# Kernel optimization log

Hardware: AMD Instinct MI355X
Metric: run time of the kernel (lower is better)

## Reference

```python
import jax, jax.numpy as jnp
import numpy as np

WS = 7
NUM_HEADS = 4
DIM = 128


def _ln(x, g, b, eps=1e-5):
    m = x.mean(-1, keepdims=True)
    v = ((x - m) ** 2).mean(-1, keepdims=True)
    return (x - m) / jnp.sqrt(v + eps) * g + b


def _rel_index(ws):
    # (N, N) relative-position index into the (2*ws-1)^2 bias table
    coords = np.stack(np.meshgrid(np.arange(ws), np.arange(ws), indexing='ij')).reshape(2, -1)
    rel = (coords[:, :, None] - coords[:, None, :]).transpose(1, 2, 0)
    rel[..., 0] += ws - 1
    rel[..., 1] += ws - 1
    rel[..., 0] *= 2 * ws - 1
    return rel.sum(-1)


def _attn_mask(Hp, Wp, ws):
    # (nW, N, N) additive shift mask, -100 where tokens come from different regions
    shift = ws // 2
    img = np.zeros((Hp, Wp))
    slices = (slice(0, -ws), slice(-ws, -shift), slice(-shift, None))
    cnt = 0
    for sh in slices:
        for sw in slices:
            img[sh, sw] = cnt
            cnt += 1
    mw = img.reshape(Hp // ws, ws, Wp // ws, ws).transpose(0, 2, 1, 3).reshape(-1, ws * ws)
    diff = mw[:, None, :] - mw[:, :, None]
    return np.where(diff != 0, -100.0, 0.0).astype(np.float32)


def setup_inputs() -> dict:
    key = jax.random.key(0)
    ks = jax.random.split(key, 8)
    d, h, ws = DIM, 4 * DIM, WS
    B, H, W = 64, 56, 56

    def w(k, shape, s=0.02):
        return (jax.random.normal(k, shape) * s).astype(jnp.float32)

    return {
        'x': jax.random.normal(ks[0], (B, H * W, d), jnp.float32),
        'norm1_g': jnp.ones(d, jnp.float32), 'norm1_b': jnp.zeros(d, jnp.float32),
        'qkv_w': w(ks[1], (d, 3 * d)), 'qkv_b': jnp.zeros(3 * d, jnp.float32),
        'proj_w': w(ks[2], (d, d)), 'proj_b': jnp.zeros(d, jnp.float32),
        'rpb_table': w(ks[3], ((2 * ws - 1) ** 2, NUM_HEADS)),
        'norm2_g': jnp.ones(d, jnp.float32), 'norm2_b': jnp.zeros(d, jnp.float32),
        'fc1_w': w(ks[4], (d, h)), 'fc1_b': jnp.zeros(h, jnp.float32),
        'fc2_w': w(ks[5], (h, d)), 'fc2_b': jnp.zeros(d, jnp.float32),
        'H': H, 'W': W,
    }


def reference(x, norm1_g, norm1_b, qkv_w, qkv_b, proj_w, proj_b, rpb_table,
              norm2_g, norm2_b, fc1_w, fc1_b, fc2_w, fc2_b, H, W):
    ws, nh = WS, NUM_HEADS
    B, L, C = x.shape
    d_head = C // nh
    scale = d_head ** -0.5
    shift = ws // 2
    N = ws * ws

    shortcut = x
    xn = _ln(x, norm1_g, norm1_b).reshape(B, H, W, C)
    pad_b = (ws - H % ws) % ws
    pad_r = (ws - W % ws) % ws
    if pad_b or pad_r:
        xn = jnp.pad(xn, ((0, 0), (0, pad_b), (0, pad_r), (0, 0)))
    Hp, Wp = H + pad_b, W + pad_r

    # cyclic shift (shift=True branch)
    xn = jnp.roll(xn, (-shift, -shift), axis=(1, 2))

    # window partition: (B, Hp, Wp, C) -> (B*nW, N, C)
    nHw, nWw = Hp // ws, Wp // ws
    win = xn.reshape(B, nHw, ws, nWw, ws, C).transpose(0, 1, 3, 2, 4, 5).reshape(B * nHw * nWw, N, C)

    qkv = (win @ qkv_w + qkv_b).reshape(-1, N, 3, nh, d_head).transpose(2, 0, 3, 1, 4)
    q, k, v = qkv[0], qkv[1], qkv[2]  # (Bw, nh, N, d_head)

    attn = jnp.einsum('bhnd,bhmd->bhnm', q, k) * scale
    bias = rpb_table[jnp.asarray(_rel_index(ws))].transpose(2, 0, 1)  # (nh, N, N)
    attn = attn + bias[None]

    mask = jnp.asarray(_attn_mask(Hp, Wp, ws))  # (nW, N, N)
    nW = mask.shape[0]
    attn = attn.reshape(B, nW, nh, N, N) + mask[None, :, None]
    attn = jax.nn.softmax(attn.reshape(-1, nh, N, N), axis=-1)

    out = jnp.einsum('bhnm,bhmd->bhnd', attn, v).transpose(0, 2, 1, 3).reshape(-1, N, C)
    out = out @ proj_w + proj_b

    # window reverse + un-shift + un-pad
    out = out.reshape(B, nHw, nWw, ws, ws, C).transpose(0, 1, 3, 2, 4, 5).reshape(B, Hp, Wp, C)
    out = jnp.roll(out, (shift, shift), axis=(1, 2))
    out = out[:, :H, :W].reshape(B, H * W, C) + shortcut

    out = out + (jax.nn.gelu(_ln(out, norm2_g, norm2_b) @ fc1_w + fc1_b, approximate=False) @ fc2_w + fc2_b)
    return out
```

## Files before the change

kernel.cpp:

```cpp
#include <hip/hip_runtime.h>
#include <hip/hip_bf16.h>
#include <math.h>

typedef __bf16 bf16x8 __attribute__((ext_vector_type(8)));
typedef __bf16 bf16x4 __attribute__((ext_vector_type(4)));
typedef float  f32x4  __attribute__((ext_vector_type(4)));
typedef unsigned int u32x4 __attribute__((ext_vector_type(4)));
typedef __hip_bfloat16 bf16_t;

static constexpr int C_    = 128;
static constexpr int L_    = 56 * 56;
static constexpr int M_    = 64 * L_;
static constexpr int NWIN  = 64 * 64;

__device__ inline long win_to_tok(int tw)
{
    int win = tw / 49, n = tw % 49;
    int bb  = win >> 6, wi = win & 63;
    int wh  = wi >> 3, wwp = wi & 7;
    int hs  = wh * 7 + n / 7;
    int wsv = wwp * 7 + n % 7;
    int hh  = (hs + 3) % 56;
    int ww  = (wsv + 3) % 56;
    return (long)bb * L_ + hh * 56 + ww;
}

__device__ inline unsigned int pk2(float lo, float hi)
{
    unsigned short a = __builtin_bit_cast(unsigned short, (__bf16)lo);
    unsigned short b = __builtin_bit_cast(unsigned short, (__bf16)hi);
    return (unsigned int)a | ((unsigned int)b << 16);
}

__device__ inline float gelu_f(float x)
{
    float u = 0.7978845608f * x * (1.f + 0.044715f * x * x);
    float e = __expf(2.f * fminf(u, 15.f));
    return x * e * __builtin_amdgcn_rcpf(e + 1.f);
}

__global__ void sentinel_kernel(float* o) { o[threadIdx.x] = 1e9f; }

__global__ void transpose_w(const float* __restrict__ w, bf16_t* __restrict__ wt,
                            int K, int N)
{
    int i = blockIdx.x * 256 + threadIdx.x;
    if (i >= K * N) return;
    int k = i / N, n = i % N;
    wt[(long)n * K + k] = __float2bfloat16(w[i]);
}

__global__ __launch_bounds__(256) void swin_fused(const float* __restrict__ x,
                                                  const float* __restrict__ lng,
                                                  const float* __restrict__ lnb,
                                                  const bf16_t* __restrict__ qkvwt,
                                                  const float*  __restrict__ qkvb,
                                                  const float*  __restrict__ rpb,
                                                  const bf16_t* __restrict__ projwt,
                                                  const float*  __restrict__ projb,
                                                  bf16_t* __restrict__ y)
{
    __shared__ char smem[16384 + 32768 + 14336];
    char*   xnb = smem;
    char*   qkb = smem + 16384;
    __bf16* vtb = (__bf16*)(smem + 49152);

    int win  = blockIdx.x;
    int tid  = threadIdx.x;
    int wave = tid >> 6;
    int lane = tid & 63;
    int la = lane & 15, lb = lane >> 4;

    for (int i = tid; i < 128 * 7; i += 256)
        vtb[(i / 7) * 56 + 49 + i % 7] = (__bf16)0.f;

    {
        int row = wave * 16 + la;
        int tw  = win * 49 + row;
        if (tw > M_ - 1) tw = M_ - 1;
        long src = win_to_tok(tw);
        const float* xr = x + src * C_;
        float vals[4][8];
        float sm = 0.f, qs = 0.f;
#pragma unroll
        for (int kt = 0; kt < 4; ++kt) {
            f32x4 u0 = *reinterpret_cast<const f32x4*>(xr + kt * 32 + lb * 8);
            f32x4 u1 = *reinterpret_cast<const f32x4*>(xr + kt * 32 + lb * 8 + 4);
#pragma unroll
            for (int j = 0; j < 4; ++j) { vals[kt][j] = u0[j]; vals[kt][4 + j] = u1[j]; }
#pragma unroll
            for (int j = 0; j < 8; ++j) { sm += vals[kt][j]; qs += vals[kt][j] * vals[kt][j]; }
        }
        sm += __shfl_xor(sm, 16); sm += __shfl_xor(sm, 32);
        qs += __shfl_xor(qs, 16); qs += __shfl_xor(qs, 32);
        float mean = sm * (1.f / 128.f);
        float rstd = rsqrtf(qs * (1.f / 128.f) - mean * mean + 1e-5f);
#pragma unroll
        for (int kt = 0; kt < 4; ++kt) {
            bf16x8 v8;
#pragma unroll
            for (int j = 0; j < 8; ++j) {
                int col = kt * 32 + lb * 8 + j;
                v8[j] = (__bf16)((vals[kt][j] - mean) * rstd * lng[col] + lnb[col]);
            }
            int colb = kt * 64 + lb * 16;
            *reinterpret_cast<bf16x8*>(xnb + row * 256 + (colb ^ ((row & 7) << 4))) = v8;
        }
    }
    __syncthreads();

    {
        int c0 = wave * 96;
        f32x4 acc[4][6];
#pragma unroll
        for (int nt = 0; nt < 6; ++nt) {
            float bv = qkvb[c0 + nt * 16 + la];
#pragma unroll
            for (int s = 0; s < 4; ++s) acc[s][nt] = (f32x4){bv, bv, bv, bv};
        }
#pragma unroll
        for (int kt = 0; kt < 4; ++kt) {
            bf16x8 ar[4];
#pragma unroll
            for (int s = 0; s < 4; ++s) {
                int row = s * 16 + la;
                ar[s] = *reinterpret_cast<const bf16x8*>(
                    xnb + row * 256 + ((kt * 64 + lb * 16) ^ ((row & 7) << 4)));
            }
#pragma unroll
            for (int nt = 0; nt < 6; ++nt) {
                bf16x8 br = *reinterpret_cast<const bf16x8*>(
                    qkvwt + (long)(c0 + nt * 16 + la) * 128 + kt * 32 + lb * 8);
#pragma unroll
                for (int s = 0; s < 4; ++s)
                    acc[s][nt] = __builtin_amdgcn_mfma_f32_16x16x32_bf16(
                        ar[s], br, acc[s][nt], 0, 0, 0);
            }
        }
#pragma unroll
        for (int s = 0; s < 4; ++s) {
#pragma unroll
            for (int r = 0; r < 4; ++r) {
                int row = s * 16 + lb * 4 + r;
#pragma unroll
                for (int nt = 0; nt < 6; ++nt) {
                    int col = c0 + nt * 16 + la;
                    float v = acc[s][nt][r];
                    if (col < 256) {
                        *reinterpret_cast<__bf16*>(
                            qkb + row * 512 + ((col * 2) ^ ((row & 7) << 4))) = (__bf16)v;
                    } else if (row < 49) {
                        vtb[(col - 256) * 56 + row] = (__bf16)v;
                    }
                }
            }
        }
    }
    __syncthreads();

    int h = wave;
    bf16x8 kf[4], qf[4];
#pragma unroll
    for (int t = 0; t < 4; ++t) {
        int row = t * 16 + la;
        kf[t] = *reinterpret_cast<const bf16x8*>(
            qkb + row * 512 + ((256 + h * 64 + lb * 16) ^ ((row & 7) << 4)));
        qf[t] = *reinterpret_cast<const bf16x8*>(
            qkb + row * 512 + ((      h * 64 + lb * 16) ^ ((row & 7) << 4)));
    }

    f32x4 S[4][4];
#pragma unroll
    for (int qt = 0; qt < 4; ++qt)
#pragma unroll
        for (int kt = 0; kt < 4; ++kt)
            S[qt][kt] = __builtin_amdgcn_mfma_f32_16x16x32_bf16(
                kf[kt], qf[qt], (f32x4){0.f, 0.f, 0.f, 0.f}, 0, 0, 0);

    const float scale = 0.17677669529663687f;
    int wi  = win & 63;
    int wh  = wi >> 3, wwp = wi & 7;
    bool edge = (wh == 7) || (wwp == 7);

    int i1[4], j1[4], r1[4], c1[4];
#pragma unroll
    for (int qt = 0; qt < 4; ++qt) {
        int q  = qt * 16 + la;
        int qc = q < 49 ? q : 48;
        i1[qt] = qc / 7; j1[qt] = qc - 7 * i1[qt];
        r1[qt] = (wh  < 7) ? 0 : ((i1[qt] < 4) ? 1 : 2);
        c1[qt] = (wwp < 7) ? 0 : ((j1[qt] < 4) ? 1 : 2);
    }

#pragma unroll
    for (int kt = 0; kt < 4; ++kt) {
#pragma unroll
        for (int r = 0; r < 4; ++r) {
            if (kt == 3 && r > 0) {
#pragma unroll
                for (int qt = 0; qt < 4; ++qt) S[qt][kt][r] = -1e30f;
                continue;
            }
            int key = kt * 16 + lb * 4 + r;
            int kc  = key < 49 ? key : 48;
            int i2  = kc / 7, j2 = kc - 7 * i2;
            int r2  = (wh  < 7) ? 0 : ((i2 < 4) ? 1 : 2);
            int c2  = (wwp < 7) ? 0 : ((j2 < 4) ? 1 : 2);
#pragma unroll
            for (int qt = 0; qt < 4; ++qt) {
                float bv  = rpb[(((i1[qt] - i2 + 6) * 13 + (j1[qt] - j2 + 6)) << 2) + h];
                float val = S[qt][kt][r] * scale + bv;
                if (edge && ((r1[qt] != r2) | (c1[qt] != c2))) val -= 100.f;
                if (kt == 3 && lb > 0) val = -1e30f;
                S[qt][kt][r] = val;
            }
        }
    }

    float inv[4];
#pragma unroll
    for (int qt = 0; qt < 4; ++qt) {
        float mx = -3e38f;
#pragma unroll
        for (int kt = 0; kt < 4; ++kt)
#pragma unroll
            for (int r = 0; r < 4; ++r) mx = fmaxf(mx, S[qt][kt][r]);
        mx = fmaxf(mx, __shfl_xor(mx, 16));
        mx = fmaxf(mx, __shfl_xor(mx, 32));
        float sm = 0.f;
#pragma unroll
        for (int kt = 0; kt < 4; ++kt)
#pragma unroll
            for (int r = 0; r < 4; ++r) {
                float e = __expf(S[qt][kt][r] - mx);
                S[qt][kt][r] = e;
                sm += e;
            }
        sm += __shfl_xor(sm, 16);
        sm += __shfl_xor(sm, 32);
        inv[qt] = 1.f / sm;
    }

    unsigned int w_[4][4][2];
#pragma unroll
    for (int qt = 0; qt < 4; ++qt)
#pragma unroll
        for (int t = 0; t < 4; ++t) {
            w_[qt][t][0] = pk2(S[qt][t][0], S[qt][t][1]);
            w_[qt][t][1] = pk2(S[qt][t][2], S[qt][t][3]);
        }

    int srcA = la + (((2 * lb)     & 3) << 4);
    int srcB = la + (((2 * lb + 1) & 3) << 4);
    bool hiT = (lb >> 1) & 1;

    f32x4 O[2][4];
#pragma unroll
    for (int dt = 0; dt < 2; ++dt)
#pragma unroll
        for (int qt = 0; qt < 4; ++qt) O[dt][qt] = (f32x4){0.f, 0.f, 0.f, 0.f};

#pragma unroll
    for (int kk = 0; kk < 2; ++kk) {
        bf16x8 vf[2];
#pragma unroll
        for (int dt = 0; dt < 2; ++dt)
            vf[dt] = *reinterpret_cast<const bf16x8*>(
                vtb + (h * 32 + dt * 16 + la) * 56 + kk * 32 + lb * 8);
        int tl = kk * 2;
#pragma unroll
        for (int qt = 0; qt < 4; ++qt) {
            unsigned int a0 = __shfl(w_[qt][tl][0],     srcA);
            unsigned int b0 = __shfl(w_[qt][tl + 1][0], srcA);
            unsigned int a1 = __shfl(w_[qt][tl][1],     srcA);
            unsigned int b1 = __shfl(w_[qt][tl + 1][1], srcA);
            unsigned int a2 = __shfl(w_[qt][tl][0],     srcB);
            unsigned int b2 = __shfl(w_[qt][tl + 1][0], srcB);
            unsigned int a3 = __shfl(w_[qt][tl][1],     srcB);
            unsigned int b3 = __shfl(w_[qt][tl + 1][1], srcB);
            u32x4 uu = { hiT ? b0 : a0, hiT ? b1 : a1, hiT ? b2 : a2, hiT ? b3 : a3 };
            bf16x8 pf = __builtin_bit_cast(bf16x8, uu);
#pragma unroll
            for (int dt = 0; dt < 2; ++dt)
                O[dt][qt] = __builtin_amdgcn_mfma_f32_16x16x32_bf16(vf[dt], pf, O[dt][qt], 0, 0, 0);
        }
    }

    __bf16 (*attw)[152] = (__bf16(*)[152])xnb;
#pragma unroll
    for (int qt = 0; qt < 4; ++qt) {
        int q = qt * 16 + la;
        if (q < 49) {
            float iv = inv[qt];
#pragma unroll
            for (int dt = 0; dt < 2; ++dt) {
                unsigned int s0 = pk2(O[dt][qt][0] * iv, O[dt][qt][1] * iv);
                unsigned int s1 = pk2(O[dt][qt][2] * iv, O[dt][qt][3] * iv);
                uint2 st = {s0, s1};
                *reinterpret_cast<uint2*>(&attw[q][h * 32 + dt * 16 + lb * 4]) = st;
            }
        }
    }
    __syncthreads();

    int n0 = h * 32;
    f32x4 pacc[4][2];
#pragma unroll
    for (int nt = 0; nt < 2; ++nt) {
        float bv = projb[n0 + nt * 16 + la];
#pragma unroll
        for (int s = 0; s < 4; ++s) pacc[s][nt] = (f32x4){bv, bv, bv, bv};
    }
#pragma unroll
    for (int kt = 0; kt < 4; ++kt) {
        bf16x8 ar[4];
#pragma unroll
        for (int s = 0; s < 4; ++s)
            ar[s] = *reinterpret_cast<const bf16x8*>(&attw[s * 16 + la][kt * 32 + lb * 8]);
#pragma unroll
        for (int nt = 0; nt < 2; ++nt) {
            bf16x8 br = *reinterpret_cast<const bf16x8*>(
                projwt + (long)(n0 + nt * 16 + la) * 128 + kt * 32 + lb * 8);
#pragma unroll
            for (int s = 0; s < 4; ++s)
                pacc[s][nt] = __builtin_amdgcn_mfma_f32_16x16x32_bf16(
                    ar[s], br, pacc[s][nt], 0, 0, 0);
        }
    }

#pragma unroll
    for (int s = 0; s < 4; ++s) {
#pragma unroll
        for (int r = 0; r < 4; ++r) {
            int q = s * 16 + lb * 4 + r;
            if (q < 49) {
                long to = win_to_tok(win * 49 + q);
#pragma unroll
                for (int nt = 0; nt < 2; ++nt) {
                    int col = n0 + nt * 16 + la;
                    y[to * C_ + col] =
                        __float2bfloat16(pacc[s][nt][r] + x[to * C_ + col]);
                }
            }
        }
    }
}

__global__ __launch_bounds__(512, 4) void mlp_fused(const bf16_t* __restrict__ y,
                                                    const float* __restrict__ g,
                                                    const float* __restrict__ b,
                                                    const bf16_t* __restrict__ w1t,
                                                    const float* __restrict__ b1,
                                                    const bf16_t* __restrict__ w2t,
                                                    const float* __restrict__ b2,
                                                    float* __restrict__ out)
{
    __shared__ uint4 ldsq[2048];
    int tid  = threadIdx.x;
    int lane = tid & 63;
    int la = lane & 15, lb = lane >> 4;
    int m0 = (blockIdx.x * 8 + (tid >> 6)) * 32;

    auto stage = [&](int c) {
        char* d1 = (char*)&ldsq[0];
        const char* s1 = (const char*)w1t + (size_t)c * 16384;
#pragma unroll
        for (int i = 0; i < 2; ++i) {
            int idx = i * 512 + tid;
            int row = idx >> 4, colb = (idx & 15) * 16;
            uint4 v = *reinterpret_cast<const uint4*>(s1 + idx * 16);
            *reinterpret_cast<uint4*>(d1 + row * 256 + (colb ^ ((row & 7) << 4))) = v;
        }
        char* d2 = (char*)&ldsq[1024];
        const char* s2 = (const char*)w2t + (size_t)c * 128;
#pragma unroll
        for (int i = 0; i < 2; ++i) {
            int idx = i * 512 + tid;
            int row = idx >> 3, colb = (idx & 7) * 16;
            uint4 v = *reinterpret_cast<const uint4*>(s2 + (size_t)row * 1024 + colb);
            *reinterpret_cast<uint4*>(d2 + row * 128 + (colb ^ ((row & 7) << 4))) = v;
        }
    };

    bf16x8 af[2][4];
#pragma unroll
    for (int s = 0; s < 2; ++s) {
        const bf16_t* yr = y + (long)(m0 + s * 16 + la) * C_;
        float vals[4][8];
        float sm = 0.f, qs = 0.f;
#pragma unroll
        for (int kt = 0; kt < 4; ++kt) {
            bf16x8 v8 = *reinterpret_cast<const bf16x8*>(yr + kt * 32 + lb * 8);
#pragma unroll
            for (int j = 0; j < 8; ++j) {
                float v = (float)v8[j];
                vals[kt][j] = v; sm += v; qs += v * v;
            }
        }
        sm += __shfl_xor(sm, 16); sm += __shfl_xor(sm, 32);
        qs += __shfl_xor(qs, 16); qs += __shfl_xor(qs, 32);
        float mean = sm * (1.f / 128.f);
        float rstd = rsqrtf(qs * (1.f / 128.f) - mean * mean + 1e-5f);
#pragma unroll
        for (int kt = 0; kt < 4; ++kt)
#pragma unroll
            for (int j = 0; j < 8; ++j) {
                int col = kt * 32 + lb * 8 + j;
                af[s][kt][j] = (__bf16)((vals[kt][j] - mean) * rstd * g[col] + b[col]);
            }
    }

    f32x4 acc[2][8];
#pragma unroll
    for (int nt2 = 0; nt2 < 8; ++nt2) {
        f32x4 bv = *reinterpret_cast<const f32x4*>(b2 + nt2 * 16 + lb * 4);
#pragma unroll
        for (int s = 0; s < 2; ++s) acc[s][nt2] = bv;
    }

    int srcA = la + (((2 * lb)     & 3) << 4);
    int srcB = la + (((2 * lb + 1) & 3) << 4);
    bool hiT = (lb >> 1) & 1;

    for (int c = 0; c < 8; ++c) {
        stage(c);
        __syncthreads();

        const char* L1 = (const char*)&ldsq[0];
        const char* L2 = (const char*)&ldsq[1024];

        f32x4 hacc[2][4];
#pragma unroll
        for (int nt = 0; nt < 4; ++nt) {
            f32x4 bv = *reinterpret_cast<const f32x4*>(b1 + c * 64 + nt * 16 + lb * 4);
#pragma unroll
            for (int s = 0; s < 2; ++s) hacc[s][nt] = bv;
        }
#pragma unroll
        for (int kt = 0; kt < 4; ++kt)
#pragma unroll
            for (int nt = 0; nt < 4; ++nt) {
                int row = nt * 16 + la;
                bf16x8 w1f = *reinterpret_cast<const bf16x8*>(
                    L1 + row * 256 + ((kt * 64 + lb * 16) ^ ((row & 7) << 4)));
#pragma unroll
                for (int s = 0; s < 2; ++s)
                    hacc[s][nt] = __builtin_amdgcn_mfma_f32_16x16x32_bf16(
                        w1f, af[s][kt], hacc[s][nt], 0, 0, 0);
            }
        unsigned int wpk[2][4][2];
#pragma unroll
        for (int s = 0; s < 2; ++s)
#pragma unroll
            for (int t = 0; t < 4; ++t) {
                f32x4 hv = hacc[s][t];
#pragma unroll
                for (int r = 0; r < 4; ++r) hv[r] = gelu_f(hv[r]);
                wpk[s][t][0] = pk2(hv[0], hv[1]);
                wpk[s][t][1] = pk2(hv[2], hv[3]);
            }
#pragma unroll
        for (int kk = 0; kk < 2; ++kk) {
            int tl = kk * 2;
#pragma unroll
            for (int s = 0; s < 2; ++s) {
                unsigned int a0 = __shfl(wpk[s][tl][0],     srcA);
                unsigned int b0 = __shfl(wpk[s][tl + 1][0], srcA);
                unsigned int a1 = __shfl(wpk[s][tl][1],     srcA);
                unsigned int b1v = __shfl(wpk[s][tl + 1][1], srcA);
                unsigned int a2 = __shfl(wpk[s][tl][0],     srcB);
                unsigned int b2v = __shfl(wpk[s][tl + 1][0], srcB);
                unsigned int a3 = __shfl(wpk[s][tl][1],     srcB);
                unsigned int b3v = __shfl(wpk[s][tl + 1][1], srcB);
                u32x4 uu = { hiT ? b0 : a0, hiT ? b1v : a1, hiT ? b2v : a2, hiT ? b3v : a3 };
                bf16x8 pf = __builtin_bit_cast(bf16x8, uu);
#pragma unroll
                for (int nt2 = 0; nt2 < 8; ++nt2) {
                    int row2 = nt2 * 16 + la;
                    bf16x8 w2f = *reinterpret_cast<const bf16x8*>(
                        L2 + row2 * 128 + ((kk * 64 + lb * 16) ^ ((row2 & 7) << 4)));
                    acc[s][nt2] = __builtin_amdgcn_mfma_f32_16x16x32_bf16(
                        w2f, pf, acc[s][nt2], 0, 0, 0);
                }
            }
        }
        __syncthreads();
    }

#pragma unroll
    for (int s = 0; s < 2; ++s) {
        long m = m0 + s * 16 + la;
        const bf16_t* yrow = y + m * C_;
        float* orow = out + m * C_;
#pragma unroll
        for (int nt2 = 0; nt2 < 8; ++nt2) {
            int n2 = nt2 * 16 + lb * 4;
            bf16x4 rb = *reinterpret_cast<const bf16x4*>(yrow + n2);
            f32x4 val = acc[s][nt2];
#pragma unroll
            for (int r = 0; r < 4; ++r) val[r] += (float)rb[r];
            *reinterpret_cast<f32x4*>(orow + n2) = val;
        }
    }
}

extern "C" void kernel_launch(void* const* d_in, const int* in_sizes, int n_in,
                              void* d_out, int out_size, void* d_ws, size_t ws_size,
                              hipStream_t stream)
{
    (void)in_sizes; (void)n_in; (void)out_size;

    const float* x      = (const float*)d_in[0];
    const float* n1g    = (const float*)d_in[1];
    const float* n1b    = (const float*)d_in[2];
    const float* qkv_w  = (const float*)d_in[3];
    const float* qkv_b  = (const float*)d_in[4];
    const float* proj_w = (const float*)d_in[5];
    const float* proj_b = (const float*)d_in[6];
    const float* rpb    = (const float*)d_in[7];
    const float* n2g    = (const float*)d_in[8];
    const float* n2b    = (const float*)d_in[9];
    const float* fc1_w  = (const float*)d_in[10];
    const float* fc1_b  = (const float*)d_in[11];
    const float* fc2_w  = (const float*)d_in[12];
    const float* fc2_b  = (const float*)d_in[13];

    char* ws = (char*)d_ws;

    const size_t yb_sz = (size_t)M_ * 128 * 2;
    const size_t w_sz  = (size_t)(128 * 384 + 128 * 128 + 128 * 512 + 512 * 128) * 2;
    const size_t need  = yb_sz + w_sz;

    if (need > ws_size) {
        sentinel_kernel<<<1, 256, 0, stream>>>((float*)d_out);
        return;
    }

    bf16_t* yb      = (bf16_t*)ws;
    bf16_t* qkv_wt  = (bf16_t*)(ws + yb_sz);
    bf16_t* proj_wt = qkv_wt + 128 * 384;
    bf16_t* fc1_wt  = proj_wt + 128 * 128;
    bf16_t* fc2_wt  = fc1_wt + 128 * 512;

    transpose_w<<<(128 * 384 + 255) / 256, 256, 0, stream>>>(qkv_w, qkv_wt, 128, 384);
    transpose_w<<<(128 * 128 + 255) / 256, 256, 0, stream>>>(proj_w, proj_wt, 128, 128);
    transpose_w<<<(128 * 512 + 255) / 256, 256, 0, stream>>>(fc1_w, fc1_wt, 128, 512);
    transpose_w<<<(512 * 128 + 255) / 256, 256, 0, stream>>>(fc2_w, fc2_wt, 512, 128);

    swin_fused<<<NWIN, 256, 0, stream>>>(x, n1g, n1b, qkv_wt, qkv_b, rpb,
                                         proj_wt, proj_b, yb);
    mlp_fused<<<M_ / 256, 512, 0, stream>>>(
        yb, n2g, n2b, fc1_wt, fc1_b, fc2_wt, fc2_b, (float*)d_out);
}
```

Baseline: 382.6 us.

## Compute per-head QKV in registers and redistribute via wave shuffles instead of LDS

Each wave now computes only its own head's Q, K and V columns, producing Q and K transposed via swapped MFMA operands. Cross-lane shuffles then repack them into MFMA operand fragments, removing the LDS round trip and the extra barrier for the qk and v buffers. Shared memory drops from about 62KB to 16KB, which may let more blocks fit per CU. The cost is extra shuffle instructions and higher register pressure, and an added barrier before the attention output reuses the LDS buffer.

```diff
diff --git a/kernel.cpp b/kernel.cpp
--- a/kernel.cpp
+++ b/kernel.cpp
@@ -60,19 +60,31 @@
                                                   const float*  __restrict__ projb,
                                                   bf16_t* __restrict__ y)
 {
-    __shared__ char smem[16384 + 32768 + 14336];
-    char*   xnb = smem;
-    char*   qkb = smem + 16384;
-    __bf16* vtb = (__bf16*)(smem + 49152);
+    __shared__ char xnb[16384];
 
     int win  = blockIdx.x;
     int tid  = threadIdx.x;
     int wave = tid >> 6;
     int lane = tid & 63;
     int la = lane & 15, lb = lane >> 4;
-
-    for (int i = tid; i < 128 * 7; i += 256)
-        vtb[(i / 7) * 56 + 49 + i % 7] = (__bf16)0.f;
+    int h = wave;
+
+    int srcA = la + (((2 * lb)     & 3) << 4);
+    int srcB = la + (((2 * lb + 1) & 3) << 4);
+    bool hiT = (lb >> 1) & 1;
+
+    auto rpk = [&](const unsigned int w0[2], const unsigned int w1[2]) -> bf16x8 {
+        unsigned int a0 = __shfl(w0[0], srcA);
+        unsigned int b0 = __shfl(w1[0], srcA);
+        unsigned int a1 = __shfl(w0[1], srcA);
+        unsigned int b1 = __shfl(w1[1], srcA);
+        unsigned int a2 = __shfl(w0[0], srcB);
+        unsigned int b2 = __shfl(w1[0], srcB);
+        unsigned int a3 = __shfl(w0[1], srcB);
+        unsigned int b3 = __shfl(w1[1], srcB);
+        u32x4 uu = { hiT ? b0 : a0, hiT ? b1 : a1, hiT ? b2 : a2, hiT ? b3 : a3 };
+        return __builtin_bit_cast(bf16x8, uu);
+    };
 
     {
         int row = wave * 16 + la;
@@ -109,64 +121,65 @@
     }
     __syncthreads();
 
-    {
-        int c0 = wave * 96;
-        f32x4 acc[4][6];
-#pragma unroll
-        for (int nt = 0; nt < 6; ++nt) {
-            float bv = qkvb[c0 + nt * 16 + la];
-#pragma unroll
-            for (int s = 0; s < 4; ++s) acc[s][nt] = (f32x4){bv, bv, bv, bv};
-        }
-#pragma unroll
-        for (int kt = 0; kt < 4; ++kt) {
-            bf16x8 ar[4];
-#pragma unroll
-            for (int s = 0; s < 4; ++s) {
-                int row = s * 16 + la;
-                ar[s] = *reinterpret_cast<const bf16x8*>(
-                    xnb + row * 256 + ((kt * 64 + lb * 16) ^ ((row & 7) << 4)));
-            }
-#pragma unroll
-            for (int nt = 0; nt < 6; ++nt) {
-                bf16x8 br = *reinterpret_cast<const bf16x8*>(
-                    qkvwt + (long)(c0 + nt * 16 + la) * 128 + kt * 32 + lb * 8);
-#pragma unroll
-                for (int s = 0; s < 4; ++s)
-                    acc[s][nt] = __builtin_amdgcn_mfma_f32_16x16x32_bf16(
-                        ar[s], br, acc[s][nt], 0, 0, 0);
-            }
-        }
-#pragma unroll
-        for (int s = 0; s < 4; ++s) {
-#pragma unroll
-            for (int r = 0; r < 4; ++r) {
-                int row = s * 16 + lb * 4 + r;
-#pragma unroll
-                for (int nt = 0; nt < 6; ++nt) {
-                    int col = c0 + nt * 16 + la;
-                    float v = acc[s][nt][r];
-                    if (col < 256) {
-                        *reinterpret_cast<__bf16*>(
-                            qkb + row * 512 + ((col * 2) ^ ((row & 7) << 4))) = (__bf16)v;
-                    } else if (row < 49) {
-                        vtb[(col - 256) * 56 + row] = (__bf16)v;
-                    }
-                }
-            }
-        }
-    }
-    __syncthreads();
-
-    int h = wave;
-    bf16x8 kf[4], qf[4];
-#pragma unroll
-    for (int t = 0; t < 4; ++t) {
-        int row = t * 16 + la;
-        kf[t] = *reinterpret_cast<const bf16x8*>(
-            qkb + row * 512 + ((256 + h * 64 + lb * 16) ^ ((row & 7) << 4)));
-        qf[t] = *reinterpret_cast<const bf16x8*>(
-            qkb + row * 512 + ((      h * 64 + lb * 16) ^ ((row & 7) << 4)));
+    f32x4 qkT[4][4];
+    f32x4 vacc[4][2];
+#pragma unroll
+    for (int ct = 0; ct < 4; ++ct) {
+        int colb = (ct < 2) ? (h * 32 + ct * 16) : (128 + h * 32 + (ct - 2) * 16);
+        f32x4 bq = *reinterpret_cast<const f32x4*>(qkvb + colb + lb * 4);
+#pragma unroll
+        for (int tt = 0; tt < 4; ++tt) qkT[ct][tt] = bq;
+    }
+#pragma unroll
+    for (int nt = 0; nt < 2; ++nt) {
+        float bv = qkvb[256 + h * 32 + nt * 16 + la];
+#pragma unroll
+        for (int s = 0; s < 4; ++s) vacc[s][nt] = (f32x4){bv, bv, bv, bv};
+    }
+
+#pragma unroll
+    for (int kt = 0; kt < 4; ++kt) {
+        bf16x8 ar[4];
+#pragma unroll
+        for (int tt = 0; tt < 4; ++tt) {
+            int row = tt * 16 + la;
+            ar[tt] = *reinterpret_cast<const bf16x8*>(
+                xnb + row * 256 + ((kt * 64 + lb * 16) ^ ((row & 7) << 4)));
+        }
+#pragma unroll
+        for (int ct = 0; ct < 4; ++ct) {
+            int colb = (ct < 2) ? (h * 32 + ct * 16) : (128 + h * 32 + (ct - 2) * 16);
+            bf16x8 wf = *reinterpret_cast<const bf16x8*>(
+                qkvwt + (long)(colb + la) * 128 + kt * 32 + lb * 8);
+#pragma unroll
+            for (int tt = 0; tt < 4; ++tt)
+                qkT[ct][tt] = __builtin_amdgcn_mfma_f32_16x16x32_bf16(
+                    wf, ar[tt], qkT[ct][tt], 0, 0, 0);
+        }
+#pragma unroll
+        for (int nt = 0; nt < 2; ++nt) {
+            bf16x8 wv = *reinterpret_cast<const bf16x8*>(
+                qkvwt + (long)(256 + h * 32 + nt * 16 + la) * 128 + kt * 32 + lb * 8);
+#pragma unroll
+            for (int s = 0; s < 4; ++s)
+                vacc[s][nt] = __builtin_amdgcn_mfma_f32_16x16x32_bf16(
+                    ar[s], wv, vacc[s][nt], 0, 0, 0);
+        }
+    }
+
+    bf16x8 qf[4], kf[4];
+#pragma unroll
+    for (int tt = 0; tt < 4; ++tt) {
+        unsigned int wq0[2] = { pk2(qkT[0][tt][0], qkT[0][tt][1]),
+                                pk2(qkT[0][tt][2], qkT[0][tt][3]) };
+        unsigned int wq1[2] = { pk2(qkT[1][tt][0], qkT[1][tt][1]),
+                                pk2(qkT[1][tt][2], qkT[1][tt][3]) };
+        qf[tt] = rpk(wq0, wq1);
+        unsigned int wk0[2] = { pk2(qkT[2][tt][0], qkT[2][tt][1]),
+                                pk2(qkT[2][tt][2], qkT[2][tt][3]) };
+        unsigned int wk1[2] = { pk2(qkT[3][tt][0], qkT[3][tt][1]),
+                                pk2(qkT[3][tt][2], qkT[3][tt][3]) };
+        kf[tt] = rpk(wk0, wk1);
     }
 
     f32x4 S[4][4];
@@ -250,9 +263,14 @@
             w_[qt][t][1] = pk2(S[qt][t][2], S[qt][t][3]);
         }
 
-    int srcA = la + (((2 * lb)     & 3) << 4);
-    int srcB = la + (((2 * lb + 1) & 3) << 4);
-    bool hiT = (lb >> 1) & 1;
+    unsigned int wvp[2][4][2];
+#pragma unroll
+    for (int nt = 0; nt < 2; ++nt)
+#pragma unroll
+        for (int s = 0; s < 4; ++s) {
+            wvp[nt][s][0] = pk2(vacc[s][nt][0], vacc[s][nt][1]);
+            wvp[nt][s][1] = pk2(vacc[s][nt][2], vacc[s][nt][3]);
+        }
 
     f32x4 O[2][4];
 #pragma unroll
@@ -262,30 +280,21 @@
 
 #pragma unroll
     for (int kk = 0; kk < 2; ++kk) {
+        int tl = kk * 2;
         bf16x8 vf[2];
 #pragma unroll
         for (int dt = 0; dt < 2; ++dt)
-            vf[dt] = *reinterpret_cast<const bf16x8*>(
-                vtb + (h * 32 + dt * 16 + la) * 56 + kk * 32 + lb * 8);
-        int tl = kk * 2;
+            vf[dt] = rpk(wvp[dt][tl], wvp[dt][tl + 1]);
 #pragma unroll
         for (int qt = 0; qt < 4; ++qt) {
-            unsigned int a0 = __shfl(w_[qt][tl][0],     srcA);
-            unsigned int b0 = __shfl(w_[qt][tl + 1][0], srcA);
-            unsigned int a1 = __shfl(w_[qt][tl][1],     srcA);
-            unsigned int b1 = __shfl(w_[qt][tl + 1][1], srcA);
-            unsigned int a2 = __shfl(w_[qt][tl][0],     srcB);
-            unsigned int b2 = __shfl(w_[qt][tl + 1][0], srcB);
-            unsigned int a3 = __shfl(w_[qt][tl][1],     srcB);
-            unsigned int b3 = __shfl(w_[qt][tl + 1][1], srcB);
-            u32x4 uu = { hiT ? b0 : a0, hiT ? b1 : a1, hiT ? b2 : a2, hiT ? b3 : a3 };
-            bf16x8 pf = __builtin_bit_cast(bf16x8, uu);
+            bf16x8 pf = rpk(w_[qt][tl], w_[qt][tl + 1]);
 #pragma unroll
             for (int dt = 0; dt < 2; ++dt)
                 O[dt][qt] = __builtin_amdgcn_mfma_f32_16x16x32_bf16(vf[dt], pf, O[dt][qt], 0, 0, 0);
         }
     }
 
+    __syncthreads();
     __bf16 (*attw)[152] = (__bf16(*)[152])xnb;
 #pragma unroll
     for (int qt = 0; qt < 4; ++qt) {
```

Result: slower. 427.4 us (+11.7%).
